# Performance work log

Hardware: AMD Instinct MI355X
Metric: run time of the kernel (lower is better)

Reference implementation:

```python
import jax, jax.numpy as jnp
import numpy as np

B, F, BOND, NFREQ, NOUT, INIT_STD = 16384, 256, 16, 4, 1, 0.1


def setup_inputs() -> dict:
    key = jax.random.key(0)
    ks = jax.random.split(key, 10)
    x = jax.random.uniform(ks[0], (B, F), dtype=jnp.float32)
    inp = {"x": x, "frequency_min": jnp.array(1.0, dtype=jnp.float32)}
    d_in = 1 + 2 * NFREQ  # physical leg dim = 9
    n, level = F, 0
    while n > 1:
        n2 = n // 2
        d_out = NOUT if n == 2 else BOND
        # stack all same-level node tensors: [n_pairs, d_left, d_right, d_out]
        inp[f"W{level}"] = jax.random.normal(ks[level + 1], (n2, d_in, d_in, d_out), dtype=jnp.float32) * INIT_STD
        d_in, n, level = d_out, n2, level + 1
    return inp


def reference(x, frequency_min, W0, W1, W2, W3, W4, W5, W6, W7):
    Ws = [W0, W1, W2, W3, W4, W5, W6, W7]
    nfreq = (W0.shape[1] - 1) // 2
    # Fourier feature map: [B, F, 1+2*nfreq]
    xs = (x * frequency_min)[..., None]
    freqs = jnp.arange(1, nfreq + 1, dtype=x.dtype)
    feats = jnp.concatenate(
        [jnp.ones_like(xs), jnp.sin(xs * freqs), jnp.cos(xs * freqs)], axis=-1
    )
    nodes = feats  # [B, n_nodes, d]
    for W in Ws:
        left = nodes[:, 0::2]   # [B, n/2, d]
        right = nodes[:, 1::2]  # [B, n/2, d]
        # batched pairwise bilinear contraction over all nodes of one level
        nodes = jnp.einsum('bni,nijd,bnj->bnd', left, W, right)
    return nodes[:, 0, :]  # [B, NOUT]
```

## Files before the change

kernel.cpp:

```cpp
#include <hip/hip_runtime.h>
#include <math.h>

#define BTOT 16384

typedef __attribute__((ext_vector_type(8))) short s16x8;
typedef __attribute__((ext_vector_type(4))) float f32x4;
typedef __attribute__((ext_vector_type(4))) uint u32x4;
typedef __attribute__((ext_vector_type(2))) float f32x2;
typedef __attribute__((ext_vector_type(2))) uint u32x2;

#define NOFF0 0u
#define NOFF1 786432u
#define NOFF2 1310720u
#define NOFF3 1572864u
#define OFF4  1703936u
#define OFF5  1769472u
#define OFF6  1802240u
#define OFF7  1818624u

__device__ __forceinline__ ushort rtn_bf16(float x) {
  uint u = __builtin_bit_cast(uint, x);
  uint r = u + 0x7fffu + ((u >> 16) & 1u);
  return (ushort)(r >> 16);
}

__global__ __launch_bounds__(256) void wprep_kernel(
    const float* __restrict__ W0, const float* __restrict__ W1,
    const float* __restrict__ W2, const float* __restrict__ W3,
    const float* __restrict__ W4, const float* __restrict__ W5,
    const float* __restrict__ W6, const float* __restrict__ W7,
    ushort* __restrict__ U) {
  __shared__ float WL[4096];
  int blk = blockIdx.x;
  if (blk < 240) {
    const float* Wsrc; ushort* dst; int din, nsrc;
    if (blk < 128)      { Wsrc = W0 + blk * 1296;         dst = U + NOFF0 + (size_t)blk * 6144;         din = 9;  nsrc = 1296; }
    else if (blk < 192) { Wsrc = W1 + (blk - 128) * 4096; dst = U + NOFF1 + (size_t)(blk - 128) * 8192; din = 16; nsrc = 4096; }
    else if (blk < 224) { Wsrc = W2 + (blk - 192) * 4096; dst = U + NOFF2 + (size_t)(blk - 192) * 8192; din = 16; nsrc = 4096; }
    else                { Wsrc = W3 + (blk - 224) * 4096; dst = U + NOFF3 + (size_t)(blk - 224) * 8192; din = 16; nsrc = 4096; }
    for (int i = threadIdx.x; i < nsrc; i += 256) WL[i] = Wsrc[i];
    __syncthreads();
    int entries = din * 256;
    for (int e = threadIdx.x; e < entries; e += 256) {
      int nt = e >> 8, l32 = (e >> 3) & 31, jj = e & 7;
      int i = ((l32 >> 4) << 3) + jj, d = l32 & 15;
      float w = (i < din) ? WL[(i * din + nt) * 16 + d] : 0.f;
      uint u = __builtin_bit_cast(uint, w);
      uint h = u & 0xffff0000u;
      dst[e] = (ushort)(h >> 16);
      dst[entries + e] = rtn_bf16(w - __builtin_bit_cast(float, h));
    }
  } else {
    const float* Wsrc; ushort* dst; int nsrc; bool dout1 = false;
    if (blk < 248)      { Wsrc = W4 + (blk - 240) * 4096; dst = U + OFF4 + (size_t)(blk - 240) * 8192; nsrc = 4096; }
    else if (blk < 252) { Wsrc = W5 + (blk - 248) * 4096; dst = U + OFF5 + (size_t)(blk - 248) * 8192; nsrc = 4096; }
    else if (blk < 254) { Wsrc = W6 + (blk - 252) * 4096; dst = U + OFF6 + (size_t)(blk - 252) * 8192; nsrc = 4096; }
    else                { Wsrc = W7;                      dst = U + OFF7;                              nsrc = 256; dout1 = true; }
    for (int i = threadIdx.x; i < nsrc; i += 256) WL[i] = Wsrc[i];
    __syncthreads();
    const int entries = 8 * 512;
    for (int e = threadIdx.x; e < entries; e += 256) {
      int kt = e >> 9, l = (e >> 3) & 63, jv = e & 7;
      int k = kt * 32 + ((l >> 4) << 3) + jv;
      int i = k >> 4, j = k & 15, n = l & 15;
      float w;
      if (dout1) w = (n == 0) ? WL[i * 16 + j] : 0.f;
      else       w = WL[(i * 16 + j) * 16 + n];
      uint u = __builtin_bit_cast(uint, w);
      uint h = u & 0xffff0000u;
      dst[e] = (ushort)(h >> 16);
      dst[entries + e] = rtn_bf16(w - __builtin_bit_cast(float, h));
    }
  }
}

__device__ __forceinline__ f32x4 split3(float li, const f32x2* rf2,
                                        s16x8 wh, s16x8 wl, f32x4 acc) {
  const f32x2 li2 = {li, li};
  u32x4 hv, lv;
#pragma unroll
  for (int jp = 0; jp < 4; ++jp) {
    f32x2 p2 = li2 * rf2[jp];
    u32x2 u2 = __builtin_bit_cast(u32x2, p2);
    u32x2 hb = u2 & 0xffff0000u;
    f32x2 h2 = __builtin_bit_cast(f32x2, hb);
    f32x2 q2 = __builtin_elementwise_fma(li2, rf2[jp], -h2);
    u32x2 uq = __builtin_bit_cast(u32x2, q2);
    hv[jp] = __builtin_amdgcn_perm(u2.y, u2.x, 0x07060302u);
    lv[jp] = __builtin_amdgcn_perm(uq.y, uq.x, 0x07060302u);
  }
  s16x8 ahi = __builtin_bit_cast(s16x8, hv);
  s16x8 alo = __builtin_bit_cast(s16x8, lv);
  acc = __builtin_amdgcn_mfma_f32_16x16x32_bf16(ahi, wh, acc, 0, 0, 0);
  acc = __builtin_amdgcn_mfma_f32_16x16x32_bf16(alo, wh, acc, 0, 0, 0);
  acc = __builtin_amdgcn_mfma_f32_16x16x32_bf16(ahi, wl, acc, 0, 0, 0);
  return acc;
}

template <int KTN, bool L0M>
__device__ __forceinline__ f32x4 mfma_core(const float* Lcol, const float* Rcol,
                                           const int ld, const ushort* __restrict__ Wf,
                                           int lane) {
  const int g = lane >> 4;
  const int j0 = (g & 1) * 8, gh = g >> 1;
  const float* Lg = Lcol + gh * ld;
  float lf[KTN];
#pragma unroll
  for (int i = 0; i < KTN; ++i)
    lf[i] = (L0M && (2 * i + gh > 8)) ? 0.f : Lg[2 * i * ld];
  f32x2 rf2[4];
#pragma unroll
  for (int j = 0; j < 8; ++j) {
    float v = (L0M && (j0 + j >= 9)) ? 0.f : Rcol[(j0 + j) * ld];
    rf2[j >> 1][j & 1] = v;
  }
  f32x4 acc = {0.f, 0.f, 0.f, 0.f};
  const int entries = KTN * 512;
#pragma unroll
  for (int kt = 0; kt < KTN; ++kt) {
    const s16x8 wh = *(const s16x8*)&Wf[(kt * 64 + lane) * 8];
    const s16x8 wl = *(const s16x8*)&Wf[entries + (kt * 64 + lane) * 8];
    acc = split3(lf[kt], rf2, wh, wl, acc);
  }
  return acc;
}

#define LDB 20

__device__ __forceinline__ void feats_row(float xv, float* Fr) {
  float s1 = __sinf(xv), c1 = __cosf(xv);
  float s2 = s1 * c1 + c1 * s1, c2 = c1 * c1 - s1 * s1;
  float s3 = s1 * c2 + c1 * s2, c3 = c1 * c2 - s1 * s2;
  float s4 = s1 * c3 + c1 * s3, c4 = c1 * c3 - s1 * s3;
  f32x4 v0 = {1.f, s1, s2, s3};
  f32x4 v1 = {s4, c1, c2, c3};
  *(f32x4*)(Fr) = v0;
  *(f32x4*)(Fr + 4) = v1;
  Fr[8] = c4;
}

template <int NT>
__device__ __forceinline__ f32x4 core2L(const float* Lb, const float* Rb,
                                        const ushort* Wl, int lane) {
  const int bb = lane & 15, g = lane >> 4;
  const ushort* whp = Wl + (lane & 31) * 8;

  const float* lp = Lb + bb * LDB + (g & 1) * 8;
  f32x4 v0 = *(const f32x4*)lp;
  f32x4 v1 = *(const f32x4*)(lp + 4);
  u32x4 u0 = __builtin_bit_cast(u32x4, v0);
  u32x4 u1 = __builtin_bit_cast(u32x4, v1);
  u32x4 hv;
  if (g < 2) {
    hv[0] = __builtin_amdgcn_perm(u0.y, u0.x, 0x07060302u);
    hv[1] = __builtin_amdgcn_perm(u0.w, u0.z, 0x07060302u);
    hv[2] = __builtin_amdgcn_perm(u1.y, u1.x, 0x07060302u);
    hv[3] = __builtin_amdgcn_perm(u1.w, u1.z, 0x07060302u);
  } else {
    u32x4 h0 = u0 & 0xffff0000u, h1 = u1 & 0xffff0000u;
    f32x4 q0 = v0 - __builtin_bit_cast(f32x4, h0);
    f32x4 q1 = v1 - __builtin_bit_cast(f32x4, h1);
    u32x4 w0 = __builtin_bit_cast(u32x4, q0), w1 = __builtin_bit_cast(u32x4, q1);
    hv[0] = __builtin_amdgcn_perm(w0.y, w0.x, 0x07060302u);
    hv[1] = __builtin_amdgcn_perm(w0.w, w0.z, 0x07060302u);
    hv[2] = __builtin_amdgcn_perm(w1.y, w1.x, 0x07060302u);
    hv[3] = __builtin_amdgcn_perm(w1.w, w1.z, 0x07060302u);
  }
  s16x8 a = __builtin_bit_cast(s16x8, hv);

  const float* rp = Rb + (g * 4) * LDB;
  f32x4 o = {0.f, 0.f, 0.f, 0.f};
  const f32x4 zz = {0.f, 0.f, 0.f, 0.f};
#pragma unroll
  for (int c = 0; c < (NT + 3) >> 2; ++c) {
    f32x4 rv0 = *(const f32x4*)(rp + c * 4);
    f32x4 rv1 = *(const f32x4*)(rp + LDB + c * 4);
    f32x4 rv2 = *(const f32x4*)(rp + 2 * LDB + c * 4);
    f32x4 rv3 = *(const f32x4*)(rp + 3 * LDB + c * 4);
#pragma unroll
    for (int jj = 0; jj < 4; ++jj) {
      const int nt = c * 4 + jj;
      if (nt < NT) {
        s16x8 wh = *(const s16x8*)(whp + nt * 256);
        s16x8 wl = *(const s16x8*)(whp + (NT + nt) * 256);
        f32x4 tt = __builtin_amdgcn_mfma_f32_16x16x32_bf16(a, wh, zz, 0, 0, 0);
        tt = __builtin_amdgcn_mfma_f32_16x16x32_bf16(a, wl, tt, 0, 0, 0);
        o[0] += rv0[jj] * tt[0];
        o[1] += rv1[jj] * tt[1];
        o[2] += rv2[jj] * tt[2];
        o[3] += rv3[jj] * tt[3];
      }
    }
  }
  return o;
}

__device__ __forceinline__ void stage_item(const ushort* gsrc, ushort* ldst,
                                           int w, int lane, int nchunks) {
#pragma unroll
  for (int c = 0; c < 4; ++c) {
    if (c < nchunks) {
      const int off = c * 4096 + w * 1024;
      __builtin_amdgcn_global_load_lds(
          (const __attribute__((address_space(1))) unsigned int*)((const char*)gsrc + off + lane * 16),
          (__attribute__((address_space(3))) unsigned int*)((char*)ldst + off),
          16, 0, 0);
    }
  }
}

constexpr int LVL15[15] = {0,0,1,0,0,1,2,0,0,1,0,0,1,2,3};
constexpr int SUB15[15] = {0,1,0,2,3,1,0,4,5,2,6,7,3,1,0};

__global__ __launch_bounds__(256, 2) void ttn_front_kernel(
    const float* __restrict__ x, const float* __restrict__ fminp,
    const ushort* __restrict__ U, float* __restrict__ s1out) {
  __shared__ float S[4][8][16 * LDB];
  __shared__ ushort WS[2][8192];
  __shared__ float XB[4][32][8];

  const int tid = threadIdx.x;
  const int lane = tid & 63, w = tid >> 6;
  const int m = lane & 15, g = lane >> 4;
  const int b0 = blockIdx.x * 64;
  const int s = blockIdx.y;
  const float fmin = fminp[0];

  float* F0 = S[w][0]; float* F1 = S[w][1];
  float* A0 = S[w][2]; float* B0 = S[w][3];
  float* A1 = S[w][4]; float* B1 = S[w][5];
  float* A2 = S[w][6]; float* B2 = S[w][7];

  if (lane < 32) {
    float* Fz = g ? F1 : F0;
    Fz[m * LDB + 9] = 0.f; Fz[m * LDB + 10] = 0.f; Fz[m * LDB + 11] = 0.f;
    *(f32x4*)(Fz + m * LDB + 12) = (f32x4){0.f, 0.f, 0.f, 0.f};
  }
  if (lane < 32) {
    const float* xrow = x + (size_t)(b0 + w * 16 + m) * 256 + s * 16;
#pragma unroll
    for (int i = 0; i < 8; ++i) XB[w][lane][i] = xrow[2 * i + g];
  }

  float* outG = s1out + (size_t)(s * 16) * BTOT + b0;

  auto storeO = [&](f32x4 a, float* Out) {
#pragma unroll
    for (int r = 0; r < 4; ++r) Out[(g * 4 + r) * LDB + m] = a[r];
  };
  auto goff = [&](int kk) -> const ushort* {
    const int l2 = LVL15[kk], s2 = SUB15[kk];
    if (l2 == 0) return U + NOFF0 + (size_t)(8 * s + s2) * 6144;
    if (l2 == 1) return U + NOFF1 + (size_t)(4 * s + s2) * 8192;
    if (l2 == 2) return U + NOFF2 + (size_t)(2 * s + s2) * 8192;
    return U + NOFF3 + (size_t)s * 8192;
  };

  stage_item(goff(0), WS[0], w, lane, 3);
  stage_item(goff(1), WS[1], w, lane, 3);

#pragma unroll
  for (int k = 0; k < 15; ++k) {
    const int lvl = LVL15[k], sub = SUB15[k];
    const int wn = (k < 14) ? (LVL15[k + 1] == 0 ? 3 : 4) : 0;
    if (wn == 3)      asm volatile("s_waitcnt vmcnt(3)" ::: "memory");
    else if (wn == 4) asm volatile("s_waitcnt vmcnt(4)" ::: "memory");
    else              asm volatile("s_waitcnt vmcnt(0)" ::: "memory");
    __builtin_amdgcn_s_barrier();
    const ushort* Wl = WS[k & 1];
    if (lvl == 0) {
      if (lane < 32) feats_row(XB[w][lane][sub] * fmin, (g ? F1 : F0) + m * LDB);
      f32x4 c = core2L<9>(F0, F1, Wl, lane);
      storeO(c, (sub & 1) ? B0 : A0);
    } else if (lvl == 1) {
      f32x4 c = core2L<16>(A0, B0, Wl, lane);
      storeO(c, (sub & 1) ? B1 : A1);
    } else if (lvl == 2) {
      f32x4 c = core2L<16>(A1, B1, Wl, lane);
      storeO(c, (sub & 1) ? B2 : A2);
    } else {
      f32x4 c = core2L<16>(A2, B2, Wl, lane);
#pragma unroll
      for (int r = 0; r < 4; ++r)
        outG[(size_t)m * BTOT + w * 16 + g * 4 + r] = c[r];
    }
    __builtin_amdgcn_s_barrier();
    if (k + 2 < 15)
      stage_item(goff(k + 2), WS[k & 1], w, lane, LVL15[k + 2] == 0 ? 3 : 4);
  }
}

__global__ __launch_bounds__(512) void ttn_back_kernel(
    const float* __restrict__ s1, const ushort* __restrict__ U,
    float* __restrict__ out) {
  __shared__ float T[256 * 17];
  __shared__ float P[8][16 * 17];
  const int tid = threadIdx.x;
  const int lane = tid & 63, v = tid >> 6;
  const int m = lane & 15, g = lane >> 4;
  const int b0 = blockIdx.x * 16;

  auto storeC = [&](f32x4 a, float* Buf) {
#pragma unroll
    for (int r = 0; r < 4; ++r) Buf[m * 17 + g * 4 + r] = a[r];
  };

#pragma unroll
  for (int it = 0; it < 2; ++it) {
    int idx = it * 512 + tid;
    int r = idx >> 2, c4 = (idx & 3) * 4;
    float4 vv = *(const float4*)&s1[(size_t)r * BTOT + b0 + c4];
    T[r * 17 + c4 + 0] = vv.x; T[r * 17 + c4 + 1] = vv.y;
    T[r * 17 + c4 + 2] = vv.z; T[r * 17 + c4 + 3] = vv.w;
  }
  __syncthreads();

  {
    f32x4 a = mfma_core<8, false>(&T[(32 * v) * 17 + m], &T[(32 * v + 16) * 17 + m],
                                  17, U + OFF4 + (size_t)v * 8192, lane);
    storeC(a, P[v]);
  }
  __syncthreads();

  if (v < 4) {
    f32x4 a = mfma_core<8, false>(&P[2 * v][m], &P[2 * v + 1][m], 17,
                                  U + OFF5 + (size_t)v * 8192, lane);
    storeC(a, &T[v * 16 * 17]);
  }
  __syncthreads();

  if (v < 2) {
    f32x4 a = mfma_core<8, false>(&T[(2 * v) * 16 * 17 + m],
                                  &T[(2 * v + 1) * 16 * 17 + m], 17,
                                  U + OFF6 + (size_t)v * 8192, lane);
    storeC(a, P[v]);
  }
  __syncthreads();

  if (v == 0) {
    f32x4 a = mfma_core<8, false>(&P[0][m], &P[1][m], 17, U + OFF7, lane);
    if (m == 0) {
#pragma unroll
      for (int r = 0; r < 4; ++r) out[b0 + g * 4 + r] = a[r];
    }
  }
}

extern "C" void kernel_launch(void* const* d_in, const int* in_sizes, int n_in,
                              void* d_out, int out_size, void* d_ws, size_t ws_size,
                              hipStream_t stream) {
  const float* x    = (const float*)d_in[0];
  const float* fmin = (const float*)d_in[1];
  const float* W0   = (const float*)d_in[2];
  const float* W1   = (const float*)d_in[3];
  const float* W2   = (const float*)d_in[4];
  const float* W3   = (const float*)d_in[5];
  const float* W4   = (const float*)d_in[6];
  const float* W5   = (const float*)d_in[7];
  const float* W6   = (const float*)d_in[8];
  const float* W7   = (const float*)d_in[9];
  float* out = (float*)d_out;

  ushort* U = (ushort*)d_ws;
  float* s1 = (float*)((char*)d_ws + (4u << 20));

  wprep_kernel<<<255, 256, 0, stream>>>(W0, W1, W2, W3, W4, W5, W6, W7, U);
  ttn_front_kernel<<<dim3(256, 16), 256, 0, stream>>>(x, fmin, U, s1);
  ttn_back_kernel<<<1024, 512, 0, stream>>>(s1, U, out);
}
```

Baseline: 249.3 us.

## Process two 16-row batch tiles per wave to reuse staged weights

```diff
diff --git a/kernel.cpp b/kernel.cpp
--- a/kernel.cpp
+++ b/kernel.cpp
@@ -139,13 +139,7 @@
   Fr[8] = c4;
 }
 
-template <int NT>
-__device__ __forceinline__ f32x4 core2L(const float* Lb, const float* Rb,
-                                        const ushort* Wl, int lane) {
-  const int bb = lane & 15, g = lane >> 4;
-  const ushort* whp = Wl + (lane & 31) * 8;
-
-  const float* lp = Lb + bb * LDB + (g & 1) * 8;
+__device__ __forceinline__ s16x8 build_a(const float* lp, int g) {
   f32x4 v0 = *(const f32x4*)lp;
   f32x4 v1 = *(const f32x4*)(lp + 4);
   u32x4 u0 = __builtin_bit_cast(u32x4, v0);
@@ -166,33 +160,55 @@
     hv[2] = __builtin_amdgcn_perm(w1.y, w1.x, 0x07060302u);
     hv[3] = __builtin_amdgcn_perm(w1.w, w1.z, 0x07060302u);
   }
-  s16x8 a = __builtin_bit_cast(s16x8, hv);
-
-  const float* rp = Rb + (g * 4) * LDB;
-  f32x4 o = {0.f, 0.f, 0.f, 0.f};
+  return __builtin_bit_cast(s16x8, hv);
+}
+
+template <int NT>
+__device__ __forceinline__ void core2L2(const float* Lb, const float* Rb,
+                                        const ushort* Wl, int lane,
+                                        f32x4& o1, f32x4& o2) {
+  const int bb = lane & 15, g = lane >> 4;
+  const ushort* whp = Wl + (lane & 31) * 8;
+
+  s16x8 a1 = build_a(Lb + bb * LDB + (g & 1) * 8, g);
+  s16x8 a2 = build_a(Lb + (16 + bb) * LDB + (g & 1) * 8, g);
+
+  const float* rp1 = Rb + (g * 4) * LDB;
+  const float* rp2 = Rb + (16 + g * 4) * LDB;
+  o1 = (f32x4){0.f, 0.f, 0.f, 0.f};
+  o2 = (f32x4){0.f, 0.f, 0.f, 0.f};
   const f32x4 zz = {0.f, 0.f, 0.f, 0.f};
 #pragma unroll
   for (int c = 0; c < (NT + 3) >> 2; ++c) {
-    f32x4 rv0 = *(const f32x4*)(rp + c * 4);
-    f32x4 rv1 = *(const f32x4*)(rp + LDB + c * 4);
-    f32x4 rv2 = *(const f32x4*)(rp + 2 * LDB + c * 4);
-    f32x4 rv3 = *(const f32x4*)(rp + 3 * LDB + c * 4);
+    f32x4 ra0 = *(const f32x4*)(rp1 + c * 4);
+    f32x4 ra1 = *(const f32x4*)(rp1 + LDB + c * 4);
+    f32x4 ra2 = *(const f32x4*)(rp1 + 2 * LDB + c * 4);
+    f32x4 ra3 = *(const f32x4*)(rp1 + 3 * LDB + c * 4);
+    f32x4 rb0 = *(const f32x4*)(rp2 + c * 4);
+    f32x4 rb1 = *(const f32x4*)(rp2 + LDB + c * 4);
+    f32x4 rb2 = *(const f32x4*)(rp2 + 2 * LDB + c * 4);
+    f32x4 rb3 = *(const f32x4*)(rp2 + 3 * LDB + c * 4);
 #pragma unroll
     for (int jj = 0; jj < 4; ++jj) {
       const int nt = c * 4 + jj;
       if (nt < NT) {
         s16x8 wh = *(const s16x8*)(whp + nt * 256);
         s16x8 wl = *(const s16x8*)(whp + (NT + nt) * 256);
-        f32x4 tt = __builtin_amdgcn_mfma_f32_16x16x32_bf16(a, wh, zz, 0, 0, 0);
-        tt = __builtin_amdgcn_mfma_f32_16x16x32_bf16(a, wl, tt, 0, 0, 0);
-        o[0] += rv0[jj] * tt[0];
-        o[1] += rv1[jj] * tt[1];
-        o[2] += rv2[jj] * tt[2];
-        o[3] += rv3[jj] * tt[3];
+        f32x4 t1 = __builtin_amdgcn_mfma_f32_16x16x32_bf16(a1, wh, zz, 0, 0, 0);
+        t1 = __builtin_amdgcn_mfma_f32_16x16x32_bf16(a1, wl, t1, 0, 0, 0);
+        f32x4 t2 = __builtin_amdgcn_mfma_f32_16x16x32_bf16(a2, wh, zz, 0, 0, 0);
+        t2 = __builtin_amdgcn_mfma_f32_16x16x32_bf16(a2, wl, t2, 0, 0, 0);
+        o1[0] += ra0[jj] * t1[0];
+        o1[1] += ra1[jj] * t1[1];
+        o1[2] += ra2[jj] * t1[2];
+        o1[3] += ra3[jj] * t1[3];
+        o2[0] += rb0[jj] * t2[0];
+        o2[1] += rb1[jj] * t2[1];
+        o2[2] += rb2[jj] * t2[2];
+        o2[3] += rb3[jj] * t2[3];
       }
     }
   }
-  return o;
 }
 
 __device__ __forceinline__ void stage_item(const ushort* gsrc, ushort* ldst,
@@ -212,17 +228,18 @@
 constexpr int LVL15[15] = {0,0,1,0,0,1,2,0,0,1,0,0,1,2,3};
 constexpr int SUB15[15] = {0,1,0,2,3,1,0,4,5,2,6,7,3,1,0};
 
-__global__ __launch_bounds__(256, 2) void ttn_front_kernel(
+__global__ __launch_bounds__(256, 1) void ttn_front_kernel(
     const float* __restrict__ x, const float* __restrict__ fminp,
     const ushort* __restrict__ U, float* __restrict__ s1out) {
-  __shared__ float S[4][8][16 * LDB];
+  __shared__ float S[4][8][32 * LDB];
   __shared__ ushort WS[2][8192];
-  __shared__ float XB[4][32][8];
+  __shared__ float XB[4][64][8];
 
   const int tid = threadIdx.x;
   const int lane = tid & 63, w = tid >> 6;
   const int m = lane & 15, g = lane >> 4;
-  const int b0 = blockIdx.x * 64;
+  const int row32 = lane & 31, side = lane >> 5;
+  const int b0 = blockIdx.x * 128;
   const int s = blockIdx.y;
   const float fmin = fminp[0];
 
@@ -231,22 +248,24 @@
   float* A1 = S[w][4]; float* B1 = S[w][5];
   float* A2 = S[w][6]; float* B2 = S[w][7];
 
-  if (lane < 32) {
-    float* Fz = g ? F1 : F0;
-    Fz[m * LDB + 9] = 0.f; Fz[m * LDB + 10] = 0.f; Fz[m * LDB + 11] = 0.f;
-    *(f32x4*)(Fz + m * LDB + 12) = (f32x4){0.f, 0.f, 0.f, 0.f};
-  }
-  if (lane < 32) {
-    const float* xrow = x + (size_t)(b0 + w * 16 + m) * 256 + s * 16;
-#pragma unroll
-    for (int i = 0; i < 8; ++i) XB[w][lane][i] = xrow[2 * i + g];
+  {
+    float* Fz = side ? F1 : F0;
+    Fz[row32 * LDB + 9] = 0.f; Fz[row32 * LDB + 10] = 0.f; Fz[row32 * LDB + 11] = 0.f;
+    *(f32x4*)(Fz + row32 * LDB + 12) = (f32x4){0.f, 0.f, 0.f, 0.f};
+  }
+  {
+    const float* xrow = x + (size_t)(b0 + w * 32 + row32) * 256 + s * 16;
+#pragma unroll
+    for (int i = 0; i < 8; ++i) XB[w][lane][i] = xrow[2 * i + side];
   }
 
   float* outG = s1out + (size_t)(s * 16) * BTOT + b0;
 
-  auto storeO = [&](f32x4 a, float* Out) {
-#pragma unroll
-    for (int r = 0; r < 4; ++r) Out[(g * 4 + r) * LDB + m] = a[r];
+  auto storeO2 = [&](const f32x4& a1v, const f32x4& a2v, float* Out) {
+#pragma unroll
+    for (int r = 0; r < 4; ++r) Out[(g * 4 + r) * LDB + m] = a1v[r];
+#pragma unroll
+    for (int r = 0; r < 4; ++r) Out[(16 + g * 4 + r) * LDB + m] = a2v[r];
   };
   auto goff = [&](int kk) -> const ushort* {
     const int l2 = LVL15[kk], s2 = SUB15[kk];
@@ -268,21 +287,25 @@
     else              asm volatile("s_waitcnt vmcnt(0)" ::: "memory");
     __builtin_amdgcn_s_barrier();
     const ushort* Wl = WS[k & 1];
+    f32x4 o1, o2;
     if (lvl == 0) {
-      if (lane < 32) feats_row(XB[w][lane][sub] * fmin, (g ? F1 : F0) + m * LDB);
-      f32x4 c = core2L<9>(F0, F1, Wl, lane);
-      storeO(c, (sub & 1) ? B0 : A0);
+      feats_row(XB[w][lane][sub] * fmin, (side ? F1 : F0) + row32 * LDB);
+      core2L2<9>(F0, F1, Wl, lane, o1, o2);
+      storeO2(o1, o2, (sub & 1) ? B0 : A0);
     } else if (lvl == 1) {
-      f32x4 c = core2L<16>(A0, B0, Wl, lane);
-      storeO(c, (sub & 1) ? B1 : A1);
+      core2L2<16>(A0, B0, Wl, lane, o1, o2);
+      storeO2(o1, o2, (sub & 1) ? B1 : A1);
     } else if (lvl == 2) {
-      f32x4 c = core2L<16>(A1, B1, Wl, lane);
-      storeO(c, (sub & 1) ? B2 : A2);
+      core2L2<16>(A1, B1, Wl, lane, o1, o2);
+      storeO2(o1, o2, (sub & 1) ? B2 : A2);
     } else {
-      f32x4 c = core2L<16>(A2, B2, Wl, lane);
+      core2L2<16>(A2, B2, Wl, lane, o1, o2);
 #pragma unroll
       for (int r = 0; r < 4; ++r)
-        outG[(size_t)m * BTOT + w * 16 + g * 4 + r] = c[r];
+        outG[(size_t)m * BTOT + w * 32 + g * 4 + r] = o1[r];
+#pragma unroll
+      for (int r = 0; r < 4; ++r)
+        outG[(size_t)m * BTOT + w * 32 + 16 + g * 4 + r] = o2[r];
     }
     __builtin_amdgcn_s_barrier();
     if (k + 2 < 15)
@@ -365,6 +388,6 @@
   float* s1 = (float*)((char*)d_ws + (4u << 20));
 
   wprep_kernel<<<255, 256, 0, stream>>>(W0, W1, W2, W3, W4, W5, W6, W7, U);
-  ttn_front_kernel<<<dim3(256, 16), 256, 0, stream>>>(x, fmin, U, s1);
+  ttn_front_kernel<<<dim3(128, 16), 256, 0, stream>>>(x, fmin, U, s1);
   ttn_back_kernel<<<1024, 512, 0, stream>>>(s1, U, out);
 }
```

Result: slower. 312.2 us (+25.2%).
